# Optimization experiments

Measured on AMD Instinct MI355X. Metric: run time of the kernel, lower is better.

The kernel has to match this reference:

```python
import jax, jax.numpy as jnp
import numpy as np

C = 1.0            # curvature
MIN_NORM = 1e-15   # hgcn min_norm
PROJ_EPS = 4e-3    # hgcn PoincareBall float32 boundary eps
N, D, E = 100000, 128, 1600000


def _artanh(x):
    # hgcn Artanh clamps input away from +-1 for stability
    return jnp.arctanh(jnp.clip(x, -1.0 + 1e-5, 1.0 - 1e-5))


def logmap0(p, c):
    sqrt_c = c ** 0.5
    p_norm = jnp.maximum(jnp.linalg.norm(p, axis=-1, keepdims=True), MIN_NORM)
    return p * _artanh(sqrt_c * p_norm) / (sqrt_c * p_norm)


def expmap0(u, c):
    sqrt_c = c ** 0.5
    u_norm = jnp.maximum(jnp.linalg.norm(u, axis=-1, keepdims=True), MIN_NORM)
    return jnp.tanh(sqrt_c * u_norm) * u / (sqrt_c * u_norm)


def proj(x, c):
    norm = jnp.maximum(jnp.linalg.norm(x, axis=-1, keepdims=True), MIN_NORM)
    maxnorm = (1.0 - PROJ_EPS) / (c ** 0.5)
    return jnp.where(norm > maxnorm, x / norm * maxnorm, x)


def setup_inputs() -> dict:
    key = jax.random.key(0)
    k1, k2, k3, k4 = jax.random.split(key, 4)
    # node features on the Poincare ball (small tangent vectors -> exp -> proj)
    x = proj(0.05 * jax.random.normal(k1, (N, D), dtype=jnp.float32), C)
    rows = jax.random.randint(k2, (E,), 0, N, dtype=jnp.int32)   # dst nodes
    cols = jax.random.randint(k3, (E,), 0, N, dtype=jnp.int32)   # src nodes
    # positive edge weights, roughly row-normalized (avg degree 16)
    vals = jax.random.uniform(k4, (E,), dtype=jnp.float32) / 16.0
    return {"x": x, "rows": rows, "cols": cols, "vals": vals}


def reference(x, rows, cols, vals):
    # x_tangent = logmap0(x)
    x_tangent = logmap0(x, C)                         # [N, D]
    # support_t = spmm(adj, x_tangent): gather src features, weight, scatter-add to dst
    msgs = vals[:, None] * x_tangent[cols]            # [E, D]
    support_t = jax.ops.segment_sum(msgs, rows, num_segments=N)  # [N, D]
    # output = proj(expmap0(support_t))
    return proj(expmap0(support_t, C), C)
```

## Files before the change

kernel.cpp:

```cpp
#include <hip/hip_runtime.h>
#include <hip/hip_fp16.h>
#include <math.h>

#define DIM 128
#define MAXNORM (1.0f - 4e-3f)
#define RPB 64
#define SUPF 8
#define SUPR (RPB * SUPF)
#define EPB 4096
#define CAP 48
#define CSTRIDE 32
#define RBLK 512
#define GTHREADS 256
#define FCAP 64

__device__ __forceinline__ float wave_reduce_sum(float v) {
    #pragma unroll
    for (int off = 32; off > 0; off >>= 1)
        v += __shfl_xor(v, off, 64);
    return v;
}

__device__ __forceinline__ unsigned pack_h2(float a, float b) {
    unsigned lo = (unsigned)__half_as_ushort(__float2half_rn(a));
    unsigned hi = (unsigned)__half_as_ushort(__float2half_rn(b));
    return lo | (hi << 16);
}

__device__ __forceinline__ float tanh_fast(float x) {
    float e = __expf(2.0f * x);
    return 1.0f - 2.0f / (e + 1.0f);
}

__global__ void xt_kernel(const float* __restrict__ x,
                          unsigned* __restrict__ xt, int n,
                          int* __restrict__ zbuf, int nz) {
    if (zbuf != nullptr) {
        int nzb = (gridDim.x < 8u) ? (int)gridDim.x : 8;
        if ((int)blockIdx.x < nzb) {
            for (int i = (int)blockIdx.x * 256 + (int)threadIdx.x; i < nz; i += nzb * 256)
                zbuf[i] = 0;
        }
    }
    int wave = (int)((blockIdx.x * blockDim.x + threadIdx.x) >> 6);
    int lane = threadIdx.x & 63;
    if (wave >= n) return;
    const float2* xr = (const float2*)(x + (size_t)wave * DIM);
    float2 v = xr[lane];
    float ss = wave_reduce_sum(v.x * v.x + v.y * v.y);
    float norm = sqrtf(ss);
    float t = fminf(norm, 1.0f - 1e-5f);
    float at = 0.5f * logf((1.0f + t) / (1.0f - t));
    float f = at / fmaxf(norm, 1e-15f);
    xt[(size_t)wave * 64 + lane] = pack_h2(v.x * f, v.y * f);
}

__global__ void partA_kernel(const int* __restrict__ rows, const int* __restrict__ cols,
                             const float* __restrict__ vals,
                             int* __restrict__ scur, uint2* __restrict__ sup,
                             int E, int NSB, int CAPS) {
    extern __shared__ int locCur[];
    int tid = threadIdx.x;
    int base = blockIdx.x * EPB;

    int er[8]; int ec[8]; float ev[8];
    #pragma unroll
    for (int k = 0; k < 8; k++) {
        int e = base + k * RBLK + tid;
        bool ok = e < E;
        er[k] = ok ? rows[e] : -1;
        ec[k] = ok ? cols[e] : 0;
        ev[k] = ok ? vals[e] : 0.f;
    }

    for (int i = tid; i < NSB; i += RBLK) locCur[i] = 0;
    __syncthreads();
    #pragma unroll
    for (int k = 0; k < 8; k++)
        if (er[k] >= 0) atomicAdd(&locCur[er[k] >> 9], 1);
    __syncthreads();
    for (int i = tid; i < NSB; i += RBLK) {
        int a = locCur[i];
        locCur[i] = a ? atomicAdd(&scur[i], a) : 0;
    }
    __syncthreads();
    #pragma unroll
    for (int k = 0; k < 8; k++) {
        if (er[k] >= 0) {
            int r = er[k];
            int s = r >> 9;
            unsigned hw = (unsigned)__half_as_ushort(__float2half(ev[k])) & 0x7fffu;
            unsigned rx = (hw << 17) | (unsigned)ec[k];
            int slot = atomicAdd(&locCur[s], 1);
            if (slot < CAPS)
                sup[(size_t)s * CAPS + slot] = make_uint2(rx, (unsigned)r);
        }
    }
}

__global__ void partB_kernel(const int* __restrict__ scur, const uint2* __restrict__ sup,
                             int* __restrict__ bcur, float* __restrict__ out,
                             int NB, int CAPS, int CAPB) {
    __shared__ int cur[SUPF];
    int s = blockIdx.x;
    int tid = threadIdx.x;
    if (tid < SUPF) cur[tid] = 0;
    __syncthreads();
    int total = scur[s]; if (total > CAPS) total = CAPS;
    const uint2* src = sup + (size_t)s * CAPS;
    for (int i = tid; i < total; i += blockDim.x) {
        uint2 rec = src[i];
        unsigned r = rec.y;
        int b = (int)(r >> 6);
        int f = b & (SUPF - 1);
        int slot = atomicAdd(&cur[f], 1);
        if (slot < CAPB) {
            uint2* recs = (uint2*)((char*)out + ((size_t)b << 15));
            recs[slot] = make_uint2(rec.x, r & (RPB - 1));
        }
    }
    __syncthreads();
    if (tid < SUPF) {
        int b = s * SUPF + tid;
        if (b < NB) bcur[b] = (cur[tid] < CAPB) ? cur[tid] : CAPB;
    }
}

__global__ void __launch_bounds__(GTHREADS, 4)
bucket_gather_kernel(const unsigned* __restrict__ xt,
                     const int* __restrict__ bcur,
                     float* __restrict__ out, int n, int CAPB) {
    __shared__ unsigned ell[RPB * CAP];
    __shared__ int cnt[RPB];
    int b = blockIdx.x;
    int tid = threadIdx.x;
    int row0 = b * RPB;
    int rowsInB = n - row0; if (rowsInB > RPB) rowsInB = RPB;
    for (int i = tid; i < RPB; i += GTHREADS) cnt[i] = 0;
    __syncthreads();
    int total = bcur[b]; if (total > CAPB) total = CAPB;
    const uint2* recs = (const uint2*)((const char*)out + ((size_t)b << 15));
    for (int i = tid; i < total; i += GTHREADS) {
        uint2 rec = recs[i];
        int lr = (int)rec.y;
        int p = atomicAdd(&cnt[lr], 1);
        if (p < CAP) ell[lr * CAP + p] = rec.x;
    }
    __syncthreads();
    if (tid < RPB) {
        int d = cnt[tid]; if (d > CAP) d = CAP;
        int dp = (d + 7) & ~7; if (dp > CAP) dp = CAP;
        for (int q = d; q < dp; ++q) ell[tid * CAP + q] = 0;
    }
    __syncthreads();
    int wv = tid >> 6, lane = tid & 63;
    unsigned lane4 = (unsigned)(lane << 2);
    for (int lr = wv; lr < rowsInB; lr += GTHREADS / 64) {
        int deg = cnt[lr]; if (deg > CAP) deg = CAP;
        float ax = 0.f, ay = 0.f;
        const unsigned* erow = &ell[lr * CAP];
        for (int j = 0; j < deg; j += 8) {
            uint4 qa = *(const uint4*)(erow + j);
            uint4 qb = *(const uint4*)(erow + j + 4);
            unsigned pk[8] = {qa.x, qa.y, qa.z, qa.w, qb.x, qb.y, qb.z, qb.w};
            __half2 u[8];
            #pragma unroll
            for (int k = 0; k < 8; k++) {
                unsigned voff = ((pk[k] & 0x1ffffu) << 8) + lane4;
                u[k] = *(const __half2*)((const char*)xt + voff);
            }
            #pragma unroll
            for (int k = 0; k < 8; k++) {
                float w = __half2float(__ushort_as_half((unsigned short)(pk[k] >> 17)));
                ax = fmaf(w, __low2float(u[k]), ax);
                ay = fmaf(w, __high2float(u[k]), ay);
            }
        }
        float ssum = wave_reduce_sum(ax * ax + ay * ay);
        float n0 = fmaxf(sqrtf(ssum), 1e-15f);
        float th = tanh_fast(n0);
        float f = (th > MAXNORM) ? (MAXNORM / n0) : (th / n0);
        float2* o = (float2*)(out + (size_t)(row0 + lr) * DIM);
        o[lane] = make_float2(ax * f, ay * f);
    }
}

__global__ void scatter_ell_kernel(const int* __restrict__ rows,
                                   const int* __restrict__ cols,
                                   const float* __restrict__ vals,
                                   int* __restrict__ cur,
                                   unsigned* __restrict__ ell, int E) {
    int e = blockIdx.x * blockDim.x + threadIdx.x;
    if (e >= E) return;
    int r = rows[e];
    unsigned hb = (unsigned)__half_as_ushort(__float2half(vals[e])) & 0x7fffu;
    unsigned pk = ((unsigned)cols[e] << 15) | hb;
    int pos = atomicAdd(&cur[(size_t)r * CSTRIDE], 1);
    if (pos < FCAP) ell[(size_t)r * FCAP + pos] = pk;
}

__global__ void gather_ell_kernel(const unsigned* __restrict__ xt,
                                  const unsigned* __restrict__ ell,
                                  const int* __restrict__ cur,
                                  float* __restrict__ out, int n) {
    int wave = (int)((blockIdx.x * blockDim.x + threadIdx.x) >> 6);
    int lane = threadIdx.x & 63;
    if (wave >= n) return;
    const __half2* xt2 = (const __half2*)xt;
    int deg = cur[(size_t)wave * CSTRIDE];
    if (deg > FCAP) deg = FCAP;
    unsigned pl = 0;
    if (lane < deg) pl = ell[(size_t)wave * FCAP + lane];
    float2 acc = make_float2(0.f, 0.f);
    for (int j = 0; j < deg; j += 8) {
        float w[8]; __half2 u[8]; int c[8];
        #pragma unroll
        for (int k = 0; k < 8; k++) {
            int idx = j + k;
            bool ok = idx < deg;
            unsigned p = __shfl(pl, ok ? idx : 0);
            c[k] = (int)(p >> 15);
            w[k] = ok ? __half2float(__ushort_as_half((unsigned short)(p & 0x7fffu))) : 0.f;
        }
        #pragma unroll
        for (int k = 0; k < 8; k++)
            u[k] = xt2[(size_t)c[k] * 64 + lane];
        #pragma unroll
        for (int k = 0; k < 8; k++) {
            acc.x = fmaf(w[k], __low2float(u[k]), acc.x);
            acc.y = fmaf(w[k], __high2float(u[k]), acc.y);
        }
    }
    float ss = wave_reduce_sum(acc.x * acc.x + acc.y * acc.y);
    float n0 = fmaxf(sqrtf(ss), 1e-15f);
    float th = tanhf(n0);
    float f = (th > MAXNORM) ? (MAXNORM / n0) : (th / n0);
    float2* o = (float2*)(out + (size_t)wave * DIM);
    o[lane] = make_float2(acc.x * f, acc.y * f);
}

__global__ void tangent_kernel(const float* __restrict__ x,
                               float* __restrict__ xt, int n) {
    int wave = (int)((blockIdx.x * blockDim.x + threadIdx.x) >> 6);
    int lane = threadIdx.x & 63;
    if (wave >= n) return;
    const float2* xr = (const float2*)(x + (size_t)wave * DIM);
    float2 v = xr[lane];
    float ss = wave_reduce_sum(v.x * v.x + v.y * v.y);
    float norm = sqrtf(ss);
    float t = fminf(norm, 1.0f - 1e-5f);
    float at = 0.5f * logf((1.0f + t) / (1.0f - t));
    float factor = at / fmaxf(norm, 1e-15f);
    float2* o = (float2*)(xt + (size_t)wave * DIM);
    o[lane] = make_float2(v.x * factor, v.y * factor);
}

__global__ void scatter_kernel(const float* __restrict__ xt,
                               const int* __restrict__ rows,
                               const int* __restrict__ cols,
                               const float* __restrict__ vals,
                               float* __restrict__ out, int E) {
    long gid = (long)blockIdx.x * blockDim.x + threadIdx.x;
    int e = (int)(gid >> 5);
    int lane = (int)(gid & 31);
    if (e >= E) return;
    int r = rows[e];
    int c = cols[e];
    float w = vals[e];
    const float4* src = (const float4*)(xt + (size_t)c * DIM);
    float4 v = src[lane];
    float* dst = out + (size_t)r * DIM + lane * 4;
    unsafeAtomicAdd(dst + 0, v.x * w);
    unsafeAtomicAdd(dst + 1, v.y * w);
    unsafeAtomicAdd(dst + 2, v.z * w);
    unsafeAtomicAdd(dst + 3, v.w * w);
}

__global__ void finalize_kernel(float* __restrict__ out, int n) {
    int wave = (int)((blockIdx.x * blockDim.x + threadIdx.x) >> 6);
    int lane = threadIdx.x & 63;
    if (wave >= n) return;
    float2* p = (float2*)(out + (size_t)wave * DIM);
    float2 v = p[lane];
    float ss = wave_reduce_sum(v.x * v.x + v.y * v.y);
    float n0 = fmaxf(sqrtf(ss), 1e-15f);
    float th = tanhf(n0);
    float factor = (th > MAXNORM) ? (MAXNORM / n0) : (th / n0);
    p[lane] = make_float2(v.x * factor, v.y * factor);
}

extern "C" void kernel_launch(void* const* d_in, const int* in_sizes, int n_in,
                              void* d_out, int out_size, void* d_ws, size_t ws_size,
                              hipStream_t stream) {
    const float* x    = (const float*)d_in[0];
    const int*   rows = (const int*)d_in[1];
    const int*   cols = (const int*)d_in[2];
    const float* vals = (const float*)d_in[3];
    float* out = (float*)d_out;

    int n = in_sizes[0] / DIM;
    int E = in_sizes[1];
    int NB  = (n + RPB - 1) / RPB;
    int NSB = (n + SUPR - 1) / SUPR;

    auto align256 = [](size_t b) { return (b + 255) & ~(size_t)255; };

    size_t xt_b = align256((size_t)n * 64 * 4);

    double fmean = (n > 0) ? (double)E * RPB / (double)n : 0.0;
    int capb = ((int)(fmean + 8.0 * sqrt(fmean + 1.0)) + 63) & ~63;
    double smean = (NSB > 0) ? (double)E / (double)NSB : 0.0;
    int caps = ((int)(smean + 8.0 * sqrt(smean + 1.0)) + 127) & ~127;
    int tail = n - (NB - 1) * RPB;

    size_t sup_b  = align256((size_t)NSB * (size_t)caps * 8);
    size_t meta_b = align256((size_t)(NSB + NB) * 4);
    size_t need   = xt_b + sup_b + meta_b;
    size_t partA_lds = (size_t)NSB * 4;

    if (n > 0 && n <= (1 << 17) && capb <= 4000 &&
        (size_t)capb * 8 <= (size_t)tail * 512 &&
        partA_lds <= 60 * 1024 && need <= ws_size) {
        unsigned* xt_h = (unsigned*)d_ws;
        uint2*    sup  = (uint2*)((char*)d_ws + xt_b);
        int*      scur = (int*)((char*)d_ws + xt_b + sup_b);
        int*      bcur = scur + NSB;

        xt_kernel<<<(n + 3) / 4, 256, 0, stream>>>(x, xt_h, n, scur, NSB + NB);
        if (E > 0) {
            int NEB = (E + EPB - 1) / EPB;
            partA_kernel<<<NEB, RBLK, partA_lds, stream>>>(rows, cols, vals,
                                                           scur, sup, E, NSB, caps);
            partB_kernel<<<NSB, RBLK, 0, stream>>>(scur, sup, bcur, out, NB, caps, capb);
        }
        bucket_gather_kernel<<<NB, GTHREADS, 0, stream>>>(xt_h, bcur, out, n, capb);
        return;
    }

    size_t ell_b = align256((size_t)n * FCAP * 4);
    size_t cur_b = align256((size_t)n * CSTRIDE * 4);
    if (n <= (1 << 17) && xt_b + ell_b + cur_b <= ws_size) {
        unsigned* xt_h = (unsigned*)d_ws;
        unsigned* ell  = (unsigned*)((char*)d_ws + xt_b);
        int*      cur  = (int*)((char*)d_ws + xt_b + ell_b);
        xt_kernel<<<(n + 3) / 4, 256, 0, stream>>>(x, xt_h, n, nullptr, 0);
        hipMemsetAsync(cur, 0, (size_t)n * CSTRIDE * 4, stream);
        scatter_ell_kernel<<<(E + 255) / 256, 256, 0, stream>>>(rows, cols, vals, cur, ell, E);
        gather_ell_kernel<<<(n + 3) / 4, 256, 0, stream>>>(xt_h, ell, cur, out, n);
        return;
    }

    float* xtf = (float*)d_in[0];
    size_t xtb = (size_t)n * DIM * sizeof(float);
    if (ws_size >= xtb) xtf = (float*)d_ws;
    tangent_kernel<<<(n + 3) / 4, 256, 0, stream>>>(x, xtf, n);
    hipMemsetAsync(d_out, 0, (size_t)n * DIM * sizeof(float), stream);
    long threads = (long)E * 32;
    scatter_kernel<<<(int)((threads + 255) / 256), 256, 0, stream>>>(xtf, rows, cols, vals, out, E);
    finalize_kernel<<<(n + 3) / 4, 256, 0, stream>>>(out, n);
}
```

Before: 215.9 us.

## Collapse two-level bucketing into single 128-row superbucket pass fused with gather

The bucketing pipeline drops from four kernels to a memset plus two kernels. The tangent-map kernel and the edge partition (partA) become one launch, with different block ranges doing each job. Superbuckets shrink to 128 rows, so the second partition pass and the bucket-gather merge into one kernel. Each block builds its ELL in LDS straight from superbucket records and then does the gather and expmap/proj. This removes the intermediate record round-trip through the output buffer and two launches, at the cost of larger static LDS (about 25KB in the gather kernel) and more global atomics on scur in partA.

```diff
diff --git a/kernel.cpp b/kernel.cpp
--- a/kernel.cpp
+++ b/kernel.cpp
@@ -4,15 +4,13 @@
 
 #define DIM 128
 #define MAXNORM (1.0f - 4e-3f)
-#define RPB 64
-#define SUPF 8
-#define SUPR (RPB * SUPF)
+#define SUPR 128
 #define EPB 4096
 #define CAP 48
 #define CSTRIDE 32
 #define RBLK 512
-#define GTHREADS 256
 #define FCAP 64
+#define MAXNSB 2048
 
 __device__ __forceinline__ float wave_reduce_sum(float v) {
     #pragma unroll
@@ -32,18 +30,53 @@
     return 1.0f - 2.0f / (e + 1.0f);
 }
 
-__global__ void xt_kernel(const float* __restrict__ x,
-                          unsigned* __restrict__ xt, int n,
-                          int* __restrict__ zbuf, int nz) {
-    if (zbuf != nullptr) {
-        int nzb = (gridDim.x < 8u) ? (int)gridDim.x : 8;
-        if ((int)blockIdx.x < nzb) {
-            for (int i = (int)blockIdx.x * 256 + (int)threadIdx.x; i < nz; i += nzb * 256)
-                zbuf[i] = 0;
-        }
-    }
-    int wave = (int)((blockIdx.x * blockDim.x + threadIdx.x) >> 6);
-    int lane = threadIdx.x & 63;
+__global__ void fused_xt_partA(const float* __restrict__ x,
+                               unsigned* __restrict__ xt, int n,
+                               const int* __restrict__ rows,
+                               const int* __restrict__ cols,
+                               const float* __restrict__ vals,
+                               int* __restrict__ scur, uint2* __restrict__ sup,
+                               int E, int NSB, int CAPS, int nA) {
+    __shared__ int locCur[MAXNSB];
+    int tid = threadIdx.x;
+    if ((int)blockIdx.x < nA) {
+        int base = blockIdx.x * EPB;
+        int er[8]; int ec[8]; float ev[8];
+        #pragma unroll
+        for (int k = 0; k < 8; k++) {
+            int e = base + k * RBLK + tid;
+            bool ok = e < E;
+            er[k] = ok ? rows[e] : -1;
+            ec[k] = ok ? cols[e] : 0;
+            ev[k] = ok ? vals[e] : 0.f;
+        }
+        for (int i = tid; i < NSB; i += RBLK) locCur[i] = 0;
+        __syncthreads();
+        #pragma unroll
+        for (int k = 0; k < 8; k++)
+            if (er[k] >= 0) atomicAdd(&locCur[er[k] >> 7], 1);
+        __syncthreads();
+        for (int i = tid; i < NSB; i += RBLK) {
+            int a = locCur[i];
+            locCur[i] = a ? atomicAdd(&scur[i], a) : 0;
+        }
+        __syncthreads();
+        #pragma unroll
+        for (int k = 0; k < 8; k++) {
+            if (er[k] >= 0) {
+                int r = er[k];
+                int s = r >> 7;
+                unsigned hw = (unsigned)__half_as_ushort(__float2half(ev[k])) & 0x7fffu;
+                unsigned rx = (hw << 17) | (unsigned)ec[k];
+                int slot = atomicAdd(&locCur[s], 1);
+                if (slot < CAPS)
+                    sup[(size_t)s * CAPS + slot] = make_uint2(rx, (unsigned)r);
+            }
+        }
+        return;
+    }
+    int wave = (int)(((blockIdx.x - nA) * RBLK + tid) >> 6);
+    int lane = tid & 63;
     if (wave >= n) return;
     const float2* xr = (const float2*)(x + (size_t)wave * DIM);
     float2 v = xr[lane];
@@ -55,99 +88,29 @@
     xt[(size_t)wave * 64 + lane] = pack_h2(v.x * f, v.y * f);
 }
 
-__global__ void partA_kernel(const int* __restrict__ rows, const int* __restrict__ cols,
-                             const float* __restrict__ vals,
-                             int* __restrict__ scur, uint2* __restrict__ sup,
-                             int E, int NSB, int CAPS) {
-    extern __shared__ int locCur[];
-    int tid = threadIdx.x;
-    int base = blockIdx.x * EPB;
-
-    int er[8]; int ec[8]; float ev[8];
-    #pragma unroll
-    for (int k = 0; k < 8; k++) {
-        int e = base + k * RBLK + tid;
-        bool ok = e < E;
-        er[k] = ok ? rows[e] : -1;
-        ec[k] = ok ? cols[e] : 0;
-        ev[k] = ok ? vals[e] : 0.f;
-    }
-
-    for (int i = tid; i < NSB; i += RBLK) locCur[i] = 0;
-    __syncthreads();
-    #pragma unroll
-    for (int k = 0; k < 8; k++)
-        if (er[k] >= 0) atomicAdd(&locCur[er[k] >> 9], 1);
-    __syncthreads();
-    for (int i = tid; i < NSB; i += RBLK) {
-        int a = locCur[i];
-        locCur[i] = a ? atomicAdd(&scur[i], a) : 0;
-    }
-    __syncthreads();
-    #pragma unroll
-    for (int k = 0; k < 8; k++) {
-        if (er[k] >= 0) {
-            int r = er[k];
-            int s = r >> 9;
-            unsigned hw = (unsigned)__half_as_ushort(__float2half(ev[k])) & 0x7fffu;
-            unsigned rx = (hw << 17) | (unsigned)ec[k];
-            int slot = atomicAdd(&locCur[s], 1);
-            if (slot < CAPS)
-                sup[(size_t)s * CAPS + slot] = make_uint2(rx, (unsigned)r);
-        }
-    }
-}
-
-__global__ void partB_kernel(const int* __restrict__ scur, const uint2* __restrict__ sup,
-                             int* __restrict__ bcur, float* __restrict__ out,
-                             int NB, int CAPS, int CAPB) {
-    __shared__ int cur[SUPF];
+__global__ void __launch_bounds__(RBLK, 8)
+partB_gather_kernel(const unsigned* __restrict__ xt,
+                    const int* __restrict__ scur,
+                    const uint2* __restrict__ sup,
+                    float* __restrict__ out, int n, int CAPS) {
+    __shared__ unsigned ell[SUPR * CAP];
+    __shared__ int cnt[SUPR];
     int s = blockIdx.x;
     int tid = threadIdx.x;
-    if (tid < SUPF) cur[tid] = 0;
+    int row0 = s * SUPR;
+    int rowsInB = n - row0; if (rowsInB > SUPR) rowsInB = SUPR;
+    for (int i = tid; i < SUPR; i += RBLK) cnt[i] = 0;
     __syncthreads();
     int total = scur[s]; if (total > CAPS) total = CAPS;
     const uint2* src = sup + (size_t)s * CAPS;
-    for (int i = tid; i < total; i += blockDim.x) {
+    for (int i = tid; i < total; i += RBLK) {
         uint2 rec = src[i];
-        unsigned r = rec.y;
-        int b = (int)(r >> 6);
-        int f = b & (SUPF - 1);
-        int slot = atomicAdd(&cur[f], 1);
-        if (slot < CAPB) {
-            uint2* recs = (uint2*)((char*)out + ((size_t)b << 15));
-            recs[slot] = make_uint2(rec.x, r & (RPB - 1));
-        }
-    }
-    __syncthreads();
-    if (tid < SUPF) {
-        int b = s * SUPF + tid;
-        if (b < NB) bcur[b] = (cur[tid] < CAPB) ? cur[tid] : CAPB;
-    }
-}
-
-__global__ void __launch_bounds__(GTHREADS, 4)
-bucket_gather_kernel(const unsigned* __restrict__ xt,
-                     const int* __restrict__ bcur,
-                     float* __restrict__ out, int n, int CAPB) {
-    __shared__ unsigned ell[RPB * CAP];
-    __shared__ int cnt[RPB];
-    int b = blockIdx.x;
-    int tid = threadIdx.x;
-    int row0 = b * RPB;
-    int rowsInB = n - row0; if (rowsInB > RPB) rowsInB = RPB;
-    for (int i = tid; i < RPB; i += GTHREADS) cnt[i] = 0;
-    __syncthreads();
-    int total = bcur[b]; if (total > CAPB) total = CAPB;
-    const uint2* recs = (const uint2*)((const char*)out + ((size_t)b << 15));
-    for (int i = tid; i < total; i += GTHREADS) {
-        uint2 rec = recs[i];
-        int lr = (int)rec.y;
+        int lr = (int)(rec.y & (SUPR - 1));
         int p = atomicAdd(&cnt[lr], 1);
         if (p < CAP) ell[lr * CAP + p] = rec.x;
     }
     __syncthreads();
-    if (tid < RPB) {
+    if (tid < SUPR) {
         int d = cnt[tid]; if (d > CAP) d = CAP;
         int dp = (d + 7) & ~7; if (dp > CAP) dp = CAP;
         for (int q = d; q < dp; ++q) ell[tid * CAP + q] = 0;
@@ -155,7 +118,7 @@
     __syncthreads();
     int wv = tid >> 6, lane = tid & 63;
     unsigned lane4 = (unsigned)(lane << 2);
-    for (int lr = wv; lr < rowsInB; lr += GTHREADS / 64) {
+    for (int lr = wv; lr < rowsInB; lr += RBLK / 64) {
         int deg = cnt[lr]; if (deg > CAP) deg = CAP;
         float ax = 0.f, ay = 0.f;
         const unsigned* erow = &ell[lr * CAP];
@@ -185,6 +148,21 @@
     }
 }
 
+__global__ void xt_kernel(const float* __restrict__ x,
+                          unsigned* __restrict__ xt, int n) {
+    int wave = (int)((blockIdx.x * blockDim.x + threadIdx.x) >> 6);
+    int lane = threadIdx.x & 63;
+    if (wave >= n) return;
+    const float2* xr = (const float2*)(x + (size_t)wave * DIM);
+    float2 v = xr[lane];
+    float ss = wave_reduce_sum(v.x * v.x + v.y * v.y);
+    float norm = sqrtf(ss);
+    float t = fminf(norm, 1.0f - 1e-5f);
+    float at = 0.5f * logf((1.0f + t) / (1.0f - t));
+    float f = at / fmaxf(norm, 1e-15f);
+    xt[(size_t)wave * 64 + lane] = pack_h2(v.x * f, v.y * f);
+}
+
 __global__ void scatter_ell_kernel(const int* __restrict__ rows,
                                    const int* __restrict__ cols,
                                    const float* __restrict__ vals,
@@ -300,40 +278,30 @@
 
     int n = in_sizes[0] / DIM;
     int E = in_sizes[1];
-    int NB  = (n + RPB - 1) / RPB;
     int NSB = (n + SUPR - 1) / SUPR;
 
     auto align256 = [](size_t b) { return (b + 255) & ~(size_t)255; };
 
     size_t xt_b = align256((size_t)n * 64 * 4);
 
-    double fmean = (n > 0) ? (double)E * RPB / (double)n : 0.0;
-    int capb = ((int)(fmean + 8.0 * sqrt(fmean + 1.0)) + 63) & ~63;
     double smean = (NSB > 0) ? (double)E / (double)NSB : 0.0;
-    int caps = ((int)(smean + 8.0 * sqrt(smean + 1.0)) + 127) & ~127;
-    int tail = n - (NB - 1) * RPB;
+    int caps = ((int)(smean + 8.0 * sqrt(smean + 1.0)) + 31) & ~31;
 
     size_t sup_b  = align256((size_t)NSB * (size_t)caps * 8);
-    size_t meta_b = align256((size_t)(NSB + NB) * 4);
+    size_t meta_b = align256((size_t)NSB * 4);
     size_t need   = xt_b + sup_b + meta_b;
-    size_t partA_lds = (size_t)NSB * 4;
-
-    if (n > 0 && n <= (1 << 17) && capb <= 4000 &&
-        (size_t)capb * 8 <= (size_t)tail * 512 &&
-        partA_lds <= 60 * 1024 && need <= ws_size) {
+
+    if (n > 0 && n <= (1 << 17) && NSB <= MAXNSB && need <= ws_size) {
         unsigned* xt_h = (unsigned*)d_ws;
         uint2*    sup  = (uint2*)((char*)d_ws + xt_b);
         int*      scur = (int*)((char*)d_ws + xt_b + sup_b);
-        int*      bcur = scur + NSB;
-
-        xt_kernel<<<(n + 3) / 4, 256, 0, stream>>>(x, xt_h, n, scur, NSB + NB);
-        if (E > 0) {
-            int NEB = (E + EPB - 1) / EPB;
-            partA_kernel<<<NEB, RBLK, partA_lds, stream>>>(rows, cols, vals,
-                                                           scur, sup, E, NSB, caps);
-            partB_kernel<<<NSB, RBLK, 0, stream>>>(scur, sup, bcur, out, NB, caps, capb);
-        }
-        bucket_gather_kernel<<<NB, GTHREADS, 0, stream>>>(xt_h, bcur, out, n, capb);
+
+        hipMemsetAsync(scur, 0, (size_t)NSB * 4, stream);
+        int nA  = (E > 0) ? (E + EPB - 1) / EPB : 0;
+        int nXt = (n * 64 + RBLK - 1) / RBLK;
+        fused_xt_partA<<<nA + nXt, RBLK, 0, stream>>>(x, xt_h, n, rows, cols, vals,
+                                                      scur, sup, E, NSB, caps, nA);
+        partB_gather_kernel<<<NSB, RBLK, 0, stream>>>(xt_h, scur, sup, out, n, caps);
         return;
     }
 
@@ -343,7 +311,7 @@
         unsigned* xt_h = (unsigned*)d_ws;
         unsigned* ell  = (unsigned*)((char*)d_ws + xt_b);
         int*      cur  = (int*)((char*)d_ws + xt_b + ell_b);
-        xt_kernel<<<(n + 3) / 4, 256, 0, stream>>>(x, xt_h, n, nullptr, 0);
+        xt_kernel<<<(n + 3) / 4, 256, 0, stream>>>(x, xt_h, n);
         hipMemsetAsync(cur, 0, (size_t)n * CSTRIDE * 4, stream);
         scatter_ell_kernel<<<(E + 255) / 256, 256, 0, stream>>>(rows, cols, vals, cur, ell, E);
         gather_ell_kernel<<<(n + 3) / 4, 256, 0, stream>>>(xt_h, ell, cur, out, n);
```

Result: faster. 208.5 us (-3.4%).
